# Kernel optimization log

Hardware: AMD Instinct MI355X
Metric: run time of the kernel (lower is better)

The kernel has to match this reference:

```python
import jax, jax.numpy as jnp
import numpy as np

NUM_TRAIN_PTS = 128
KNN = 32
KNN_CLEAN = 4
SIGMA = 0.01
FEAT_DIM = 128
B, N, M = 2, 40000, 40000


def knn_gather(query, pts, k):
    """Brute-force KNN. query [B,Q,3], pts [B,P,3] -> neighbors [B,Q,k,3]."""
    # squared euclidean distances [B,Q,P]
    d2 = (jnp.sum(query * query, -1, keepdims=True)
          - 2.0 * jnp.einsum('bqd,bpd->bqp', query, pts)
          + jnp.sum(pts * pts, -1)[:, None, :])
    _, idx = jax.lax.top_k(-d2, k)                # [B,Q,k]
    nn = jax.vmap(lambda p, i: p[i])(pts, idx)    # gather -> [B,Q,k,3]
    return nn


def setup_inputs() -> dict:
    key = jax.random.key(0)
    k0, k1, k2, k3, k4, k5 = jax.random.split(key, 6)
    noisy_pc = jax.random.uniform(k0, (B, N, 3), dtype=jnp.float32)
    clean_pc = jax.random.uniform(k1, (B, M, 3), dtype=jnp.float32)
    sampled_idx = jax.random.randint(k2, (NUM_TRAIN_PTS,), 0, N)
    Wf = jax.random.normal(k3, (3, FEAT_DIM), dtype=jnp.float32) * 0.1
    Wx = jax.random.normal(k4, (3, 3), dtype=jnp.float32) * 0.1
    Wc = jax.random.normal(k5, (FEAT_DIM, 3), dtype=jnp.float32) * 0.1
    return {'noisy_pc': noisy_pc, 'clean_pc': clean_pc, 'sampled_idx': sampled_idx,
            'Wf': Wf, 'Wx': Wx, 'Wc': Wc}


def reference(noisy_pc, clean_pc, sampled_idx, Wf, Wx, Wc):
    P, K, Kc = NUM_TRAIN_PTS, KNN, KNN_CLEAN
    # per-point feature extraction (stand-in for FeatureExtraction), then sample
    noisy_feat = jnp.einsum('bnd,df->bnf', noisy_pc, Wf)[:, sampled_idx, :]  # [B,P,F]
    q = noisy_pc[:, sampled_idx, :]                                          # [B,P,3]
    # first KNN: neighbors of sampled points within the noisy cloud
    f = knn_gather(q, noisy_pc, K)                                           # [B,P,K,3]
    # score network (stand-in): local offsets + conditioning feature
    estim_score = (jnp.einsum('bpkd,de->bpke', f - q[:, :, None, :], Wx)
                   + jnp.einsum('bpf,fe->bpe', noisy_feat, Wc)[:, :, None, :])  # [B,P,K,3]
    # second KNN: each neighbor point vs the clean cloud (clean shared per batch,
    # avoiding the torch .repeat of clean_pc per training point)
    knn_clean = knn_gather(f.reshape(f.shape[0], P * K, 3), clean_pc, Kc)
    knn_clean = knn_clean.reshape(f.shape[0], P, K, Kc, 3)                   # [B,P,K,Kc,3]
    ground_score = -jnp.mean(f[:, :, :, None, :] - knn_clean, axis=3)        # [B,P,K,3]
    loss = 0.5 * jnp.mean(jnp.sum((estim_score - ground_score) ** 2 * (1.0 / SIGMA), axis=-1))
    return loss
```

## Files before the change

kernel.cpp:

```cpp
#include <hip/hip_runtime.h>
#include <hip/hip_bf16.h>

#define N_PTS   40000
#define N_B     2
#define N_P     128
#define N_K     32
#define N_KC    4
#define N_FEAT  128
#define NQ2     (N_B * N_P * N_K)
#define BIGF    3.0e38f

#define K1SUB   8
#define K1RANGE (N_PTS / K1SUB)
#define QCAP1   512
#define LBUF1   320

#define QCAP    96

#define TAU2    4.0e-3f
#define TAU1    1.6e-2f

#define NG      15
#define NCELL   (NG * NG * NG)
#define GB_BLK  20
#define GB_PER  (N_PTS / GB_BLK)

#define NLOSSB  2048

__device__ int    g_sidx[N_P];
__device__ int    g_fidx[NQ2];
__device__ int    g_q1cnt[256];
__device__ unsigned long long g_q1list[256 * QCAP1];
__device__ int    g_bincnt[N_B * NCELL];
__device__ int    g_binstart[N_B * (NCELL + 1)];
__device__ int    g_cursor[N_B * NCELL];
__device__ float4 g_cpts[N_B * N_PTS];
__device__ int    g_cpidx[N_B * N_PTS];
__device__ float  g_lploss[NLOSSB];
__device__ float  g_M3[9];
__device__ float  g_WxS[9];

__device__ __forceinline__ int clampi(int v, int lo, int hi) { return v < lo ? lo : (v > hi ? hi : v); }

__device__ __forceinline__ unsigned long long packkey(float d, int idx)
{
    unsigned int u = __float_as_uint(d);
    u ^= (u >> 31) ? 0xFFFFFFFFu : 0x80000000u;
    return ((unsigned long long)u << 32) | (unsigned int)idx;
}

__device__ __forceinline__ int cell_of(float x, float y, float z)
{
    const int cx = clampi((int)(x * NG), 0, NG - 1);
    const int cy = clampi((int)(y * NG), 0, NG - 1);
    const int cz = clampi((int)(z * NG), 0, NG - 1);
    return cx + NG * (cy + NG * cz);
}

__global__ __launch_bounds__(256) void setup_kernel(
    const float* __restrict__ clean,
    const void*  __restrict__ sidx_raw,
    const float* __restrict__ Wf,
    const float* __restrict__ Wx,
    const float* __restrict__ Wc)
{
    __shared__ int hist[NCELL];
    __shared__ int flags[4];
    const int blk = blockIdx.x;
    const int tid = threadIdx.x;

    if (blk < N_B * GB_BLK) {
        const int bb = blk / GB_BLK;
        const int sb = blk % GB_BLK;
        const float* cb = clean + bb * (N_PTS * 3);

        for (int i = tid; i < NCELL; i += 256) hist[i] = 0;
        __syncthreads();

        const int j0 = sb * GB_PER;
        for (int j = j0 + tid; j < j0 + GB_PER; j += 256) {
            const float x = cb[j * 3 + 0], y = cb[j * 3 + 1], z = cb[j * 3 + 2];
            atomicAdd(&hist[cell_of(x, y, z)], 1);
        }
        __syncthreads();

        for (int i = tid; i < NCELL; i += 256) {
            const int v = hist[i];
            if (v) atomicAdd(&g_bincnt[bb * NCELL + i], v);
        }
    } else {
        if (tid < 9) {
            const int d = tid / 3, e = tid % 3;
            float acc = 0.0f;
            for (int f0 = 0; f0 < N_FEAT; ++f0)
                acc += Wf[d * N_FEAT + f0] * Wc[f0 * 3 + e];
            g_M3[tid]  = acc;
            g_WxS[tid] = Wx[tid];
        }
        if (tid == 0) { flags[0] = 1; flags[1] = 1; flags[2] = 1; flags[3] = 1; }
        __syncthreads();
        const int*       p32 = (const int*)sidx_raw;
        const long long* p64 = (const long long*)sidx_raw;
        const float*     pf  = (const float*)sidx_raw;
        if (tid < 128) {
            const int       v32 = p32[tid];
            const long long v64 = p64[tid];
            const float     vf  = pf[tid];
            if (!(v32 >= 0 && v32 < N_PTS)) atomicAnd(&flags[0], 0);
            if ((tid & 1) && v32 != 0)      atomicAnd(&flags[1], 0);
            if (!(v64 >= 0 && v64 < N_PTS)) atomicAnd(&flags[2], 0);
            if (!(vf >= 0.0f && vf < (float)N_PTS && vf == floorf(vf))) atomicAnd(&flags[3], 0);
        }
        __syncthreads();
        if (tid < 128) {
            int si;
            if (flags[0] && !(flags[1] && flags[2])) si = p32[tid];
            else if (flags[2])                       si = (int)p64[tid];
            else if (flags[3])                       si = (int)(pf[tid] + 0.5f);
            else                                     si = 0;
            g_sidx[tid] = clampi(si, 0, N_PTS - 1);
        }
    }
}

__global__ __launch_bounds__(256) void scan_knn1_kernel(
    const float* __restrict__ noisy)
{
    __shared__ unsigned long long buf[LBUF1];
    __shared__ int lcnt;
    __shared__ int base_s;
    __shared__ int wsum[4], woff[4];
    const int blk = blockIdx.x;
    const int tid = threadIdx.x;

    if (blk < N_B) {
        const int bb   = blk;
        const int lane = tid & 63, wv = tid >> 6;

        int lvals[14];
        int lsum = 0;
#pragma unroll
        for (int t = 0; t < 14; ++t) {
            const int idx = tid * 14 + t;
            lvals[t] = (idx < NCELL) ? g_bincnt[bb * NCELL + idx] : 0;
            lsum += lvals[t];
        }
        int v = lsum;
#pragma unroll
        for (int off = 1; off < 64; off <<= 1) {
            const int n = __shfl_up(v, off);
            if (lane >= off) v += n;
        }
        if (lane == 63) wsum[wv] = v;
        __syncthreads();
        if (tid == 0) { int r = 0; for (int w = 0; w < 4; ++w) { woff[w] = r; r += wsum[w]; } }
        __syncthreads();

        int run = woff[wv] + (v - lsum);
#pragma unroll
        for (int t = 0; t < 14; ++t) {
            const int idx = tid * 14 + t;
            if (idx < NCELL) {
                g_binstart[bb * (NCELL + 1) + idx] = run;
                g_cursor[bb * NCELL + idx] = run;
                g_bincnt[bb * NCELL + idx] = 0;
                run += lvals[t];
            }
        }
        if (tid == 0) g_binstart[bb * (NCELL + 1) + NCELL] = N_PTS;
    } else {
        const int idx = blk - N_B;
        const int qb  = idx & 255;
        const int sub = idx >> 8;
        const int b   = qb >> 7;
        const int p   = qb & 127;
        const float* nb = noisy + b * (N_PTS * 3);

        if (tid == 0) lcnt = 0;
        const int si = g_sidx[p];
        const float qx = nb[si * 3 + 0];
        const float qy = nb[si * 3 + 1];
        const float qz = nb[si * 3 + 2];
        __syncthreads();

        const int jbeg = sub * K1RANGE;
        const int jend = jbeg + K1RANGE;
        for (int j = jbeg + tid; j < jend; j += 256) {
            const float dx = qx - nb[j * 3 + 0];
            const float dy = qy - nb[j * 3 + 1];
            const float dz = qz - nb[j * 3 + 2];
            const float d2 = fmaf(dz, dz, fmaf(dy, dy, dx * dx));
            if (d2 < TAU1) {
                const int slot = atomicAdd(&lcnt, 1);
                if (slot < LBUF1)
                    buf[slot] = ((unsigned long long)__float_as_uint(d2) << 32) | (unsigned int)j;
            }
        }
        __syncthreads();

        const int cnt = lcnt;
        if (tid == 0) {
            const int add = (cnt <= LBUF1) ? cnt : (QCAP1 + 1000);
            base_s = atomicAdd(&g_q1cnt[qb], add);
        }
        __syncthreads();

        const int base = base_s;
        const int n = (cnt < LBUF1) ? cnt : LBUF1;
        for (int i = tid; i < n; i += 256) {
            const int o = base + i;
            if (o < QCAP1) g_q1list[qb * QCAP1 + o] = buf[i];
        }
    }
}

__global__ __launch_bounds__(256) void merge_scatter_kernel(
    const float* __restrict__ noisy,
    const float* __restrict__ clean)
{
    __shared__ unsigned long long keys[2048];
    const int blk = blockIdx.x;
    const int tid = threadIdx.x;

    if (blk >= 256) {
        const int idx = blk - 256;
        const int bb  = idx / GB_BLK;
        const int sb  = idx % GB_BLK;
        const float* cb = clean + bb * (N_PTS * 3);

        const int j0 = sb * GB_PER;
        for (int j = j0 + tid; j < j0 + GB_PER; j += 256) {
            const float x = cb[j * 3 + 0], y = cb[j * 3 + 1], z = cb[j * 3 + 2];
            const int c = cell_of(x, y, z);
            const int pos = atomicAdd(&g_cursor[bb * NCELL + c], 1);
            const float pp = fmaf(z, z, fmaf(y, y, x * x));
            g_cpts[bb * N_PTS + pos]  = make_float4(x, y, z, pp);
            g_cpidx[bb * N_PTS + pos] = j;
        }
        return;
    }

    const int qb  = blk;
    const int cnt = g_q1cnt[qb];

    if (cnt >= 32 && cnt <= QCAP1) {
        for (int i = tid; i < QCAP1; i += 256)
            keys[i] = (i < cnt) ? g_q1list[qb * QCAP1 + i] : ~0ULL;
        __syncthreads();
        for (int k = 2; k <= QCAP1; k <<= 1) {
            for (int jj = k >> 1; jj > 0; jj >>= 1) {
                const int idx = tid;
                const int i = ((idx & ~(jj - 1)) << 1) | (idx & (jj - 1));
                const int partner = i | jj;
                const bool asc = ((i & k) == 0);
                const unsigned long long a = keys[i];
                const unsigned long long c = keys[partner];
                if ((a > c) == asc) { keys[i] = c; keys[partner] = a; }
                __syncthreads();
            }
        }
    } else {
        const int b = qb >> 7;
        const float* nb = noisy + b * (N_PTS * 3);
        const int si = g_sidx[qb & 127];
        const float qx = nb[si * 3 + 0];
        const float qy = nb[si * 3 + 1];
        const float qz = nb[si * 3 + 2];

        float bd[8]; int bi[8];
#pragma unroll
        for (int i = 0; i < 8; ++i) { bd[i] = BIGF; bi[i] = 0x7fffffff; }
        for (int j = tid; j < N_PTS; j += 256) {
            const float dx = qx - nb[j * 3 + 0];
            const float dy = qy - nb[j * 3 + 1];
            const float dz = qz - nb[j * 3 + 2];
            const float d2 = fmaf(dz, dz, fmaf(dy, dy, dx * dx));
            if (d2 < bd[7]) {
                bd[7] = d2; bi[7] = j;
#pragma unroll
                for (int t = 7; t > 0; --t) {
                    if (bd[t] < bd[t - 1]) {
                        float td = bd[t]; bd[t] = bd[t - 1]; bd[t - 1] = td;
                        int   ti = bi[t]; bi[t] = bi[t - 1]; bi[t - 1] = ti;
                    }
                }
            }
        }
#pragma unroll
        for (int t = 0; t < 8; ++t)
            keys[tid * 8 + t] = ((unsigned long long)__float_as_uint(bd[t]) << 32)
                              | (unsigned int)bi[t];
        __syncthreads();
        for (int k = 2; k <= 2048; k <<= 1) {
            for (int jj = k >> 1; jj > 0; jj >>= 1) {
#pragma unroll
                for (int base = 0; base < 2048; base += 256) {
                    const int i = base + tid;
                    const int partner = i ^ jj;
                    if (partner > i) {
                        const bool asc = ((i & k) == 0);
                        const unsigned long long a = keys[i];
                        const unsigned long long c = keys[partner];
                        if ((a > c) == asc) { keys[i] = c; keys[partner] = a; }
                    }
                }
                __syncthreads();
            }
        }
    }

    if (tid < 32) {
        const int idx = (int)(keys[tid] & 0xFFFFFFFFull);
        g_fidx[qb * 32 + tid] = clampi(idx, 0, N_PTS - 1);
    }
    if (tid == 0) g_q1cnt[qb] = 0;
}

__global__ __launch_bounds__(256) void knn2_loss_kernel(
    const float* __restrict__ noisy,
    const float* __restrict__ clean)
{
    __shared__ float2 buf[4][QCAP];
    __shared__ int    bcnt[4];
    __shared__ float  red[4];
    const int tid  = threadIdx.x;
    const int wv   = tid >> 6;
    const int lane = tid & 63;
    const int g    = blockIdx.x * 4 + wv;
    const int b    = g >> 12;
    const int p    = (g >> 5) & 127;
    const float* nb = noisy + b * (N_PTS * 3);
    const float* cb = clean + b * (N_PTS * 3);

    if (lane == 0) bcnt[wv] = 0;

    const int fid = clampi(g_fidx[g], 0, N_PTS - 1);
    const float fx = nb[fid * 3 + 0];
    const float fy = nb[fid * 3 + 1];
    const float fz = nb[fid * 3 + 2];
    const float fm2x = -2.0f * fx, fm2y = -2.0f * fy, fm2z = -2.0f * fz;
    const float ff = fmaf(fz, fz, fmaf(fy, fy, fx * fx));
    const float taup = TAU2 - ff;

    const int cfx = clampi((int)(fx * NG), 0, NG - 1);
    const int cfy = clampi((int)(fy * NG), 0, NG - 1);
    const int cfz = clampi((int)(fz * NG), 0, NG - 1);
    const int bso = b * (NCELL + 1);
    const int bpo = b * N_PTS;

    if (lane < 27) {
        const int cx = cfx + (lane % 3) - 1;
        const int cy = cfy + ((lane / 3) % 3) - 1;
        const int cz = cfz + (lane / 9) - 1;
        if (cx >= 0 && cx < NG && cy >= 0 && cy < NG && cz >= 0 && cz < NG) {
            const int c = cx + NG * (cy + NG * cz);
            const int s = g_binstart[bso + c];
            const int e = g_binstart[bso + c + 1];
            for (int k = s; k < e; ++k) {
                const float4 pt = g_cpts[bpo + k];
                const float d2 = fmaf(fm2x, pt.x, fmaf(fm2y, pt.y, fmaf(fm2z, pt.z, pt.w)));
                if (d2 < taup) {
                    const int slot = atomicAdd(&bcnt[wv], 1);
                    if (slot < QCAP)
                        buf[wv][slot] = make_float2(d2, __int_as_float(g_cpidx[bpo + k]));
                }
            }
        }
    }
    __syncthreads();

    const int cnt = bcnt[wv];
    int nn[4];

    if (cnt >= 4 && cnt <= QCAP) {
        unsigned long long e0 = ~0ULL, e1 = ~0ULL;
        if (lane < cnt) {
            const float2 a = buf[wv][lane];
            e0 = packkey(a.x, __float_as_int(a.y));
        }
        if (lane + 64 < cnt) {
            const float2 a = buf[wv][lane + 64];
            e1 = packkey(a.x, __float_as_int(a.y));
        }
        if (e1 < e0) { unsigned long long t = e0; e0 = e1; e1 = t; }

        int c = 0;
#pragma unroll
        for (int r = 0; r < 4; ++r) {
            const unsigned long long h = (c == 0) ? e0 : ((c == 1) ? e1 : ~0ULL);
            unsigned long long m = h;
#pragma unroll
            for (int off = 32; off; off >>= 1) {
                const unsigned long long o = __shfl_xor(m, off);
                if (o < m) m = o;
            }
            if (h == m) c++;
            nn[r] = (int)(m & 0xFFFFFFFFull);
        }
    } else {
        float bd[4]; int bi[4];
#pragma unroll
        for (int t = 0; t < 4; ++t) { bd[t] = BIGF; bi[t] = 0x7fffffff; }
        for (int j = lane; j < N_PTS; j += 64) {
            const float dx = fx - cb[j * 3 + 0];
            const float dy = fy - cb[j * 3 + 1];
            const float dz = fz - cb[j * 3 + 2];
            const float d2 = fmaf(dz, dz, fmaf(dy, dy, dx * dx));
            if (d2 < bd[3]) {
                bd[3] = d2; bi[3] = j;
#pragma unroll
                for (int t = 3; t > 0; --t) {
                    if (bd[t] < bd[t - 1]) {
                        float td = bd[t]; bd[t] = bd[t - 1]; bd[t - 1] = td;
                        int   ti = bi[t]; bi[t] = bi[t - 1]; bi[t - 1] = ti;
                    }
                }
            }
        }
        int cur = 0;
        for (int r = 0; r < 4; ++r) {
            float v  = (cur < 4) ? bd[cur] : BIGF;
            int   vi = (cur < 4) ? bi[cur] : 0x7fffffff;
            int   who = lane;
#pragma unroll
            for (int off = 32; off; off >>= 1) {
                const float v2  = __shfl_down(v, off);
                const int   vi2 = __shfl_down(vi, off);
                const int   w2  = __shfl_down(who, off);
                if (v2 < v || (v2 == v && vi2 < vi)) { v = v2; vi = vi2; who = w2; }
            }
            const int bvi = __shfl(vi, 0);
            const int bwh = __shfl(who, 0);
            nn[r] = bvi;
            if (lane == bwh) cur++;
        }
    }

    float t2 = 0.0f;
    if (lane == 0) {
        const int si = g_sidx[p];
        const float qx = nb[si * 3 + 0], qy = nb[si * 3 + 1], qz = nb[si * 3 + 2];
        const int n0 = clampi(nn[0], 0, N_PTS - 1), n1 = clampi(nn[1], 0, N_PTS - 1);
        const int n2 = clampi(nn[2], 0, N_PTS - 1), n3 = clampi(nn[3], 0, N_PTS - 1);
        const float mx = 0.25f * (cb[n0*3+0] + cb[n1*3+0] + cb[n2*3+0] + cb[n3*3+0]);
        const float my = 0.25f * (cb[n0*3+1] + cb[n1*3+1] + cb[n2*3+1] + cb[n3*3+1]);
        const float mz = 0.25f * (cb[n0*3+2] + cb[n1*3+2] + cb[n2*3+2] + cb[n3*3+2]);

        const float gx = mx - fx, gy = my - fy, gz = mz - fz;
        const float rx = fx - qx, ry = fy - qy, rz = fz - qz;
        const float ex = rx * g_WxS[0] + ry * g_WxS[3] + rz * g_WxS[6] + qx * g_M3[0] + qy * g_M3[3] + qz * g_M3[6];
        const float ey = rx * g_WxS[1] + ry * g_WxS[4] + rz * g_WxS[7] + qx * g_M3[1] + qy * g_M3[4] + qz * g_M3[7];
        const float ez = rx * g_WxS[2] + ry * g_WxS[5] + rz * g_WxS[8] + qx * g_M3[2] + qy * g_M3[5] + qz * g_M3[8];
        const float dx = ex - gx, dy = ey - gy, dz = ez - gz;
        t2 = dx * dx + dy * dy + dz * dz;
    }

    if (lane == 0) red[wv] = t2;
    __syncthreads();
    if (tid == 0) g_lploss[blockIdx.x] = (red[0] + red[1]) + (red[2] + red[3]);
}

__global__ __launch_bounds__(256) void final_kernel(float* __restrict__ out)
{
    __shared__ float red[4];
    const int tid = threadIdx.x;
    float v = 0.0f;
    for (int i = tid; i < NLOSSB; i += 256) v += g_lploss[i];
#pragma unroll
    for (int off = 32; off; off >>= 1) v += __shfl_down(v, off);
    if ((tid & 63) == 0) red[tid >> 6] = v;
    __syncthreads();
    if (tid == 0) out[0] = ((red[0] + red[1]) + (red[2] + red[3])) * (50.0f / 8192.0f);
}

extern "C" void kernel_launch(void* const* d_in, const int* in_sizes, int n_in,
                              void* d_out, int out_size, void* d_ws, size_t ws_size,
                              hipStream_t stream)
{
    (void)d_ws; (void)ws_size; (void)in_sizes; (void)n_in; (void)out_size;

    const float* noisy = (const float*)d_in[0];
    const float* clean = (const float*)d_in[1];
    const float* Wf    = (const float*)d_in[3];
    const float* Wx    = (const float*)d_in[4];
    const float* Wc    = (const float*)d_in[5];

    setup_kernel<<<N_B * GB_BLK + 1, 256, 0, stream>>>(clean, d_in[2], Wf, Wx, Wc);
    scan_knn1_kernel<<<N_B + 256 * K1SUB, 256, 0, stream>>>(noisy);
    merge_scatter_kernel<<<256 + N_B * GB_BLK, 256, 0, stream>>>(noisy, clean);
    knn2_loss_kernel<<<NLOSSB, 256, 0, stream>>>(noisy, clean);
    final_kernel<<<1, 256, 0, stream>>>((float*)d_out);
}
```

Measured before the change: 112.4 us.

## Fuse pipeline stages using last-block-done atomics to cut kernel launches

Cuts the launch sequence from five kernels to three by using a global atomic counter in each stage, so the last finishing block does the follow-on work. The prefix scan of the grid histogram moves into the last histogram block, the per-query merge/sort into the last of its KNN1 sub-blocks, and the final loss reduction into the last knn2 block. This removes launch gaps and inter-kernel drains. In exchange it adds fences and atomics, and the last-block tails run serially on a single block.

Result: slower. 401.1 us (+257.0%).

```diff
diff --git a/kernel.cpp b/kernel.cpp
--- a/kernel.cpp
+++ b/kernel.cpp
@@ -39,6 +39,9 @@
 __device__ float  g_lploss[NLOSSB];
 __device__ float  g_M3[9];
 __device__ float  g_WxS[9];
+__device__ int    g_histdone[N_B];
+__device__ int    g_q1done[256];
+__device__ int    g_lossdone;
 
 __device__ __forceinline__ int clampi(int v, int lo, int hi) { return v < lo ? lo : (v > hi ? hi : v); }
 
@@ -66,6 +69,8 @@
 {
     __shared__ int hist[NCELL];
     __shared__ int flags[4];
+    __shared__ int wsum[4], woff[4];
+    __shared__ int islast;
     const int blk = blockIdx.x;
     const int tid = threadIdx.x;
 
@@ -87,6 +92,49 @@
         for (int i = tid; i < NCELL; i += 256) {
             const int v = hist[i];
             if (v) atomicAdd(&g_bincnt[bb * NCELL + i], v);
+        }
+
+        __threadfence();
+        __syncthreads();
+        if (tid == 0) islast = (atomicAdd(&g_histdone[bb], 1) == GB_BLK - 1);
+        __syncthreads();
+        if (!islast) return;
+        __threadfence();
+
+        const int lane = tid & 63, wv = tid >> 6;
+        int lvals[14];
+        int lsum = 0;
+#pragma unroll
+        for (int t = 0; t < 14; ++t) {
+            const int idx = tid * 14 + t;
+            lvals[t] = (idx < NCELL) ? g_bincnt[bb * NCELL + idx] : 0;
+            lsum += lvals[t];
+        }
+        int v = lsum;
+#pragma unroll
+        for (int off = 1; off < 64; off <<= 1) {
+            const int n = __shfl_up(v, off);
+            if (lane >= off) v += n;
+        }
+        if (lane == 63) wsum[wv] = v;
+        __syncthreads();
+        if (tid == 0) { int r = 0; for (int w = 0; w < 4; ++w) { woff[w] = r; r += wsum[w]; } }
+        __syncthreads();
+
+        int run = woff[wv] + (v - lsum);
+#pragma unroll
+        for (int t = 0; t < 14; ++t) {
+            const int idx = tid * 14 + t;
+            if (idx < NCELL) {
+                g_binstart[bb * (NCELL + 1) + idx] = run;
+                g_cursor[bb * NCELL + idx] = run;
+                g_bincnt[bb * NCELL + idx] = 0;
+                run += lvals[t];
+            }
+        }
+        if (tid == 0) {
+            g_binstart[bb * (NCELL + 1) + NCELL] = N_PTS;
+            g_histdone[bb] = 0;
         }
     } else {
         if (tid < 9) {
@@ -123,109 +171,18 @@
     }
 }
 
-__global__ __launch_bounds__(256) void scan_knn1_kernel(
-    const float* __restrict__ noisy)
-{
-    __shared__ unsigned long long buf[LBUF1];
-    __shared__ int lcnt;
-    __shared__ int base_s;
-    __shared__ int wsum[4], woff[4];
+__global__ __launch_bounds__(256) void knn1_scatter_kernel(
+    const float* __restrict__ noisy,
+    const float* __restrict__ clean)
+{
+    __shared__ unsigned long long skey[2048];
+    __shared__ int lcnt, base_s, islast;
     const int blk = blockIdx.x;
     const int tid = threadIdx.x;
 
-    if (blk < N_B) {
-        const int bb   = blk;
-        const int lane = tid & 63, wv = tid >> 6;
-
-        int lvals[14];
-        int lsum = 0;
-#pragma unroll
-        for (int t = 0; t < 14; ++t) {
-            const int idx = tid * 14 + t;
-            lvals[t] = (idx < NCELL) ? g_bincnt[bb * NCELL + idx] : 0;
-            lsum += lvals[t];
-        }
-        int v = lsum;
-#pragma unroll
-        for (int off = 1; off < 64; off <<= 1) {
-            const int n = __shfl_up(v, off);
-            if (lane >= off) v += n;
-        }
-        if (lane == 63) wsum[wv] = v;
-        __syncthreads();
-        if (tid == 0) { int r = 0; for (int w = 0; w < 4; ++w) { woff[w] = r; r += wsum[w]; } }
-        __syncthreads();
-
-        int run = woff[wv] + (v - lsum);
-#pragma unroll
-        for (int t = 0; t < 14; ++t) {
-            const int idx = tid * 14 + t;
-            if (idx < NCELL) {
-                g_binstart[bb * (NCELL + 1) + idx] = run;
-                g_cursor[bb * NCELL + idx] = run;
-                g_bincnt[bb * NCELL + idx] = 0;
-                run += lvals[t];
-            }
-        }
-        if (tid == 0) g_binstart[bb * (NCELL + 1) + NCELL] = N_PTS;
-    } else {
-        const int idx = blk - N_B;
-        const int qb  = idx & 255;
-        const int sub = idx >> 8;
-        const int b   = qb >> 7;
-        const int p   = qb & 127;
-        const float* nb = noisy + b * (N_PTS * 3);
-
-        if (tid == 0) lcnt = 0;
-        const int si = g_sidx[p];
-        const float qx = nb[si * 3 + 0];
-        const float qy = nb[si * 3 + 1];
-        const float qz = nb[si * 3 + 2];
-        __syncthreads();
-
-        const int jbeg = sub * K1RANGE;
-        const int jend = jbeg + K1RANGE;
-        for (int j = jbeg + tid; j < jend; j += 256) {
-            const float dx = qx - nb[j * 3 + 0];
-            const float dy = qy - nb[j * 3 + 1];
-            const float dz = qz - nb[j * 3 + 2];
-            const float d2 = fmaf(dz, dz, fmaf(dy, dy, dx * dx));
-            if (d2 < TAU1) {
-                const int slot = atomicAdd(&lcnt, 1);
-                if (slot < LBUF1)
-                    buf[slot] = ((unsigned long long)__float_as_uint(d2) << 32) | (unsigned int)j;
-            }
-        }
-        __syncthreads();
-
-        const int cnt = lcnt;
-        if (tid == 0) {
-            const int add = (cnt <= LBUF1) ? cnt : (QCAP1 + 1000);
-            base_s = atomicAdd(&g_q1cnt[qb], add);
-        }
-        __syncthreads();
-
-        const int base = base_s;
-        const int n = (cnt < LBUF1) ? cnt : LBUF1;
-        for (int i = tid; i < n; i += 256) {
-            const int o = base + i;
-            if (o < QCAP1) g_q1list[qb * QCAP1 + o] = buf[i];
-        }
-    }
-}
-
-__global__ __launch_bounds__(256) void merge_scatter_kernel(
-    const float* __restrict__ noisy,
-    const float* __restrict__ clean)
-{
-    __shared__ unsigned long long keys[2048];
-    const int blk = blockIdx.x;
-    const int tid = threadIdx.x;
-
-    if (blk >= 256) {
-        const int idx = blk - 256;
-        const int bb  = idx / GB_BLK;
-        const int sb  = idx % GB_BLK;
+    if (blk < N_B * GB_BLK) {
+        const int bb = blk / GB_BLK;
+        const int sb = blk % GB_BLK;
         const float* cb = clean + bb * (N_PTS * 3);
 
         const int j0 = sb * GB_PER;
@@ -240,33 +197,74 @@
         return;
     }
 
-    const int qb  = blk;
+    const int idx = blk - N_B * GB_BLK;
+    const int qb  = idx & 255;
+    const int sub = idx >> 8;
+    const int b   = qb >> 7;
+    const int p   = qb & 127;
+    const float* nb = noisy + b * (N_PTS * 3);
+
+    if (tid == 0) lcnt = 0;
+    const int si = g_sidx[p];
+    const float qx = nb[si * 3 + 0];
+    const float qy = nb[si * 3 + 1];
+    const float qz = nb[si * 3 + 2];
+    __syncthreads();
+
+    const int jbeg = sub * K1RANGE;
+    const int jend = jbeg + K1RANGE;
+    for (int j = jbeg + tid; j < jend; j += 256) {
+        const float dx = qx - nb[j * 3 + 0];
+        const float dy = qy - nb[j * 3 + 1];
+        const float dz = qz - nb[j * 3 + 2];
+        const float d2 = fmaf(dz, dz, fmaf(dy, dy, dx * dx));
+        if (d2 < TAU1) {
+            const int slot = atomicAdd(&lcnt, 1);
+            if (slot < LBUF1)
+                skey[slot] = ((unsigned long long)__float_as_uint(d2) << 32) | (unsigned int)j;
+        }
+    }
+    __syncthreads();
+
+    const int scnt = lcnt;
+    if (tid == 0) {
+        const int add = (scnt <= LBUF1) ? scnt : (QCAP1 + 1000);
+        base_s = atomicAdd(&g_q1cnt[qb], add);
+    }
+    __syncthreads();
+
+    const int base = base_s;
+    const int nout = (scnt < LBUF1) ? scnt : LBUF1;
+    for (int i = tid; i < nout; i += 256) {
+        const int o = base + i;
+        if (o < QCAP1) g_q1list[qb * QCAP1 + o] = skey[i];
+    }
+
+    __threadfence();
+    __syncthreads();
+    if (tid == 0) islast = (atomicAdd(&g_q1done[qb], 1) == K1SUB - 1);
+    __syncthreads();
+    if (!islast) return;
+    __threadfence();
+
     const int cnt = g_q1cnt[qb];
 
     if (cnt >= 32 && cnt <= QCAP1) {
         for (int i = tid; i < QCAP1; i += 256)
-            keys[i] = (i < cnt) ? g_q1list[qb * QCAP1 + i] : ~0ULL;
+            skey[i] = (i < cnt) ? g_q1list[qb * QCAP1 + i] : ~0ULL;
         __syncthreads();
         for (int k = 2; k <= QCAP1; k <<= 1) {
             for (int jj = k >> 1; jj > 0; jj >>= 1) {
-                const int idx = tid;
-                const int i = ((idx & ~(jj - 1)) << 1) | (idx & (jj - 1));
+                const int i = ((tid & ~(jj - 1)) << 1) | (tid & (jj - 1));
                 const int partner = i | jj;
                 const bool asc = ((i & k) == 0);
-                const unsigned long long a = keys[i];
-                const unsigned long long c = keys[partner];
-                if ((a > c) == asc) { keys[i] = c; keys[partner] = a; }
+                const unsigned long long a = skey[i];
+                const unsigned long long c = skey[partner];
+                if ((a > c) == asc) { skey[i] = c; skey[partner] = a; }
                 __syncthreads();
             }
         }
     } else {
-        const int b = qb >> 7;
-        const float* nb = noisy + b * (N_PTS * 3);
-        const int si = g_sidx[qb & 127];
-        const float qx = nb[si * 3 + 0];
-        const float qy = nb[si * 3 + 1];
-        const float qz = nb[si * 3 + 2];
-
         float bd[8]; int bi[8];
 #pragma unroll
         for (int i = 0; i < 8; ++i) { bd[i] = BIGF; bi[i] = 0x7fffffff; }
@@ -288,20 +286,20 @@
         }
 #pragma unroll
         for (int t = 0; t < 8; ++t)
-            keys[tid * 8 + t] = ((unsigned long long)__float_as_uint(bd[t]) << 32)
+            skey[tid * 8 + t] = ((unsigned long long)__float_as_uint(bd[t]) << 32)
                               | (unsigned int)bi[t];
         __syncthreads();
         for (int k = 2; k <= 2048; k <<= 1) {
             for (int jj = k >> 1; jj > 0; jj >>= 1) {
 #pragma unroll
-                for (int base = 0; base < 2048; base += 256) {
-                    const int i = base + tid;
+                for (int bas = 0; bas < 2048; bas += 256) {
+                    const int i = bas + tid;
                     const int partner = i ^ jj;
                     if (partner > i) {
                         const bool asc = ((i & k) == 0);
-                        const unsigned long long a = keys[i];
-                        const unsigned long long c = keys[partner];
-                        if ((a > c) == asc) { keys[i] = c; keys[partner] = a; }
+                        const unsigned long long a = skey[i];
+                        const unsigned long long c = skey[partner];
+                        if ((a > c) == asc) { skey[i] = c; skey[partner] = a; }
                     }
                 }
                 __syncthreads();
@@ -310,19 +308,21 @@
     }
 
     if (tid < 32) {
-        const int idx = (int)(keys[tid] & 0xFFFFFFFFull);
-        g_fidx[qb * 32 + tid] = clampi(idx, 0, N_PTS - 1);
-    }
-    if (tid == 0) g_q1cnt[qb] = 0;
+        const int fi = (int)(skey[tid] & 0xFFFFFFFFull);
+        g_fidx[qb * 32 + tid] = clampi(fi, 0, N_PTS - 1);
+    }
+    if (tid == 0) { g_q1cnt[qb] = 0; g_q1done[qb] = 0; }
 }
 
 __global__ __launch_bounds__(256) void knn2_loss_kernel(
     const float* __restrict__ noisy,
-    const float* __restrict__ clean)
+    const float* __restrict__ clean,
+    float* __restrict__ out)
 {
     __shared__ float2 buf[4][QCAP];
     __shared__ int    bcnt[4];
     __shared__ float  red[4];
+    __shared__ int    islast;
     const int tid  = threadIdx.x;
     const int wv   = tid >> 6;
     const int lane = tid & 63;
@@ -458,19 +458,24 @@
     if (lane == 0) red[wv] = t2;
     __syncthreads();
     if (tid == 0) g_lploss[blockIdx.x] = (red[0] + red[1]) + (red[2] + red[3]);
-}
-
-__global__ __launch_bounds__(256) void final_kernel(float* __restrict__ out)
-{
-    __shared__ float red[4];
-    const int tid = threadIdx.x;
+
+    __threadfence();
+    __syncthreads();
+    if (tid == 0) islast = (atomicAdd(&g_lossdone, 1) == NLOSSB - 1);
+    __syncthreads();
+    if (!islast) return;
+    __threadfence();
+
     float v = 0.0f;
     for (int i = tid; i < NLOSSB; i += 256) v += g_lploss[i];
 #pragma unroll
     for (int off = 32; off; off >>= 1) v += __shfl_down(v, off);
     if ((tid & 63) == 0) red[tid >> 6] = v;
     __syncthreads();
-    if (tid == 0) out[0] = ((red[0] + red[1]) + (red[2] + red[3])) * (50.0f / 8192.0f);
+    if (tid == 0) {
+        out[0] = ((red[0] + red[1]) + (red[2] + red[3])) * (50.0f / 8192.0f);
+        g_lossdone = 0;
+    }
 }
 
 extern "C" void kernel_launch(void* const* d_in, const int* in_sizes, int n_in,
@@ -486,8 +491,6 @@
     const float* Wc    = (const float*)d_in[5];
 
     setup_kernel<<<N_B * GB_BLK + 1, 256, 0, stream>>>(clean, d_in[2], Wf, Wx, Wc);
-    scan_knn1_kernel<<<N_B + 256 * K1SUB, 256, 0, stream>>>(noisy);
-    merge_scatter_kernel<<<256 + N_B * GB_BLK, 256, 0, stream>>>(noisy, clean);
-    knn2_loss_kernel<<<NLOSSB, 256, 0, stream>>>(noisy, clean);
-    final_kernel<<<1, 256, 0, stream>>>((float*)d_out);
-}
+    knn1_scatter_kernel<<<N_B * GB_BLK + 256 * K1SUB, 256, 0, stream>>>(noisy, clean);
+    knn2_loss_kernel<<<NLOSSB, 256, 0, stream>>>(noisy, clean, (float*)d_out);
+}
```

## Replace brute-force KNN1 scan and prefix-sum binning with fixed-capacity grid buckets

Applied to the files above, without the earlier changes.

Builds a coarse 7^3 grid over the noisy cloud and fixed-capacity buckets for the clean-cloud grid with direct atomic slot insertion, replacing the histogram plus prefix-scan plus scatter pipeline. The first KNN now scans only the 27 neighbouring coarse cells instead of all 40000 points, and candidate selection is fused into the same kernel, removing one launch and the global candidate list. Counter resets move into extra blocks of the final kernel. The change relies on bucket capacities not overflowing; when they do, it falls back to the existing slower paths.

Result: no change. 114.3 us (+1.8%).

```diff
diff --git a/kernel.cpp b/kernel.cpp
--- a/kernel.cpp
+++ b/kernel.cpp
@@ -10,11 +10,7 @@
 #define NQ2     (N_B * N_P * N_K)
 #define BIGF    3.0e38f
 
-#define K1SUB   8
-#define K1RANGE (N_PTS / K1SUB)
 #define QCAP1   512
-#define LBUF1   320
-
 #define QCAP    96
 
 #define TAU2    4.0e-3f
@@ -22,6 +18,12 @@
 
 #define NG      15
 #define NCELL   (NG * NG * NG)
+#define CAPC    32
+
+#define NG1     7
+#define NCELL1  (NG1 * NG1 * NG1)
+#define CAP1N   192
+
 #define GB_BLK  20
 #define GB_PER  (N_PTS / GB_BLK)
 
@@ -29,13 +31,11 @@
 
 __device__ int    g_sidx[N_P];
 __device__ int    g_fidx[NQ2];
-__device__ int    g_q1cnt[256];
-__device__ unsigned long long g_q1list[256 * QCAP1];
-__device__ int    g_bincnt[N_B * NCELL];
-__device__ int    g_binstart[N_B * (NCELL + 1)];
-__device__ int    g_cursor[N_B * NCELL];
-__device__ float4 g_cpts[N_B * N_PTS];
-__device__ int    g_cpidx[N_B * N_PTS];
+__device__ int    g_ncnt[N_B * NCELL1];
+__device__ float4 g_npts[N_B * NCELL1 * CAP1N];
+__device__ int    g_ccnt[N_B * NCELL];
+__device__ float4 g_cpts[N_B * NCELL * CAPC];
+__device__ int    g_cpidx[N_B * NCELL * CAPC];
 __device__ float  g_lploss[NLOSSB];
 __device__ float  g_M3[9];
 __device__ float  g_WxS[9];
@@ -57,14 +57,14 @@
     return cx + NG * (cy + NG * cz);
 }
 
-__global__ __launch_bounds__(256) void setup_kernel(
+__global__ __launch_bounds__(256) void build_kernel(
+    const float* __restrict__ noisy,
     const float* __restrict__ clean,
     const void*  __restrict__ sidx_raw,
     const float* __restrict__ Wf,
     const float* __restrict__ Wx,
     const float* __restrict__ Wc)
 {
-    __shared__ int hist[NCELL];
     __shared__ int flags[4];
     const int blk = blockIdx.x;
     const int tid = threadIdx.x;
@@ -72,21 +72,33 @@
     if (blk < N_B * GB_BLK) {
         const int bb = blk / GB_BLK;
         const int sb = blk % GB_BLK;
+        const float* nb = noisy + bb * (N_PTS * 3);
+        const int j0 = sb * GB_PER;
+        for (int j = j0 + tid; j < j0 + GB_PER; j += 256) {
+            const float x = nb[j * 3 + 0], y = nb[j * 3 + 1], z = nb[j * 3 + 2];
+            const int cx = clampi((int)(x * NG1), 0, NG1 - 1);
+            const int cy = clampi((int)(y * NG1), 0, NG1 - 1);
+            const int cz = clampi((int)(z * NG1), 0, NG1 - 1);
+            const int ci = bb * NCELL1 + cx + NG1 * (cy + NG1 * cz);
+            const int pos = atomicAdd(&g_ncnt[ci], 1);
+            if (pos < CAP1N)
+                g_npts[ci * CAP1N + pos] = make_float4(x, y, z, __int_as_float(j));
+        }
+    } else if (blk < 2 * N_B * GB_BLK) {
+        const int blk2 = blk - N_B * GB_BLK;
+        const int bb = blk2 / GB_BLK;
+        const int sb = blk2 % GB_BLK;
         const float* cb = clean + bb * (N_PTS * 3);
-
-        for (int i = tid; i < NCELL; i += 256) hist[i] = 0;
-        __syncthreads();
-
         const int j0 = sb * GB_PER;
         for (int j = j0 + tid; j < j0 + GB_PER; j += 256) {
             const float x = cb[j * 3 + 0], y = cb[j * 3 + 1], z = cb[j * 3 + 2];
-            atomicAdd(&hist[cell_of(x, y, z)], 1);
-        }
-        __syncthreads();
-
-        for (int i = tid; i < NCELL; i += 256) {
-            const int v = hist[i];
-            if (v) atomicAdd(&g_bincnt[bb * NCELL + i], v);
+            const int ci = bb * NCELL + cell_of(x, y, z);
+            const int pos = atomicAdd(&g_ccnt[ci], 1);
+            if (pos < CAPC) {
+                const float pp = fmaf(z, z, fmaf(y, y, x * x));
+                g_cpts[ci * CAPC + pos]  = make_float4(x, y, z, pp);
+                g_cpidx[ci * CAPC + pos] = j;
+            }
         }
     } else {
         if (tid < 9) {
@@ -123,134 +135,63 @@
     }
 }
 
-__global__ __launch_bounds__(256) void scan_knn1_kernel(
+__global__ __launch_bounds__(256) void knn1_grid_kernel(
     const float* __restrict__ noisy)
 {
-    __shared__ unsigned long long buf[LBUF1];
-    __shared__ int lcnt;
-    __shared__ int base_s;
-    __shared__ int wsum[4], woff[4];
-    const int blk = blockIdx.x;
-    const int tid = threadIdx.x;
-
-    if (blk < N_B) {
-        const int bb   = blk;
-        const int lane = tid & 63, wv = tid >> 6;
-
-        int lvals[14];
-        int lsum = 0;
-#pragma unroll
-        for (int t = 0; t < 14; ++t) {
-            const int idx = tid * 14 + t;
-            lvals[t] = (idx < NCELL) ? g_bincnt[bb * NCELL + idx] : 0;
-            lsum += lvals[t];
-        }
-        int v = lsum;
-#pragma unroll
-        for (int off = 1; off < 64; off <<= 1) {
-            const int n = __shfl_up(v, off);
-            if (lane >= off) v += n;
-        }
-        if (lane == 63) wsum[wv] = v;
-        __syncthreads();
-        if (tid == 0) { int r = 0; for (int w = 0; w < 4; ++w) { woff[w] = r; r += wsum[w]; } }
-        __syncthreads();
-
-        int run = woff[wv] + (v - lsum);
-#pragma unroll
-        for (int t = 0; t < 14; ++t) {
-            const int idx = tid * 14 + t;
-            if (idx < NCELL) {
-                g_binstart[bb * (NCELL + 1) + idx] = run;
-                g_cursor[bb * NCELL + idx] = run;
-                g_bincnt[bb * NCELL + idx] = 0;
-                run += lvals[t];
-            }
-        }
-        if (tid == 0) g_binstart[bb * (NCELL + 1) + NCELL] = N_PTS;
-    } else {
-        const int idx = blk - N_B;
-        const int qb  = idx & 255;
-        const int sub = idx >> 8;
-        const int b   = qb >> 7;
-        const int p   = qb & 127;
-        const float* nb = noisy + b * (N_PTS * 3);
-
-        if (tid == 0) lcnt = 0;
-        const int si = g_sidx[p];
-        const float qx = nb[si * 3 + 0];
-        const float qy = nb[si * 3 + 1];
-        const float qz = nb[si * 3 + 2];
-        __syncthreads();
-
-        const int jbeg = sub * K1RANGE;
-        const int jend = jbeg + K1RANGE;
-        for (int j = jbeg + tid; j < jend; j += 256) {
-            const float dx = qx - nb[j * 3 + 0];
-            const float dy = qy - nb[j * 3 + 1];
-            const float dz = qz - nb[j * 3 + 2];
+    __shared__ unsigned long long keys[2048];
+    __shared__ int lcnt, ovf;
+    const int qb   = blockIdx.x;
+    const int tid  = threadIdx.x;
+    const int wv   = tid >> 6;
+    const int lane = tid & 63;
+    const int b    = qb >> 7;
+    const int p    = qb & 127;
+    const float* nb = noisy + b * (N_PTS * 3);
+
+    if (tid == 0) { lcnt = 0; ovf = 0; }
+    const int si = g_sidx[p];
+    const float qx = nb[si * 3 + 0];
+    const float qy = nb[si * 3 + 1];
+    const float qz = nb[si * 3 + 2];
+    const int c1x = clampi((int)(qx * NG1), 0, NG1 - 1);
+    const int c1y = clampi((int)(qy * NG1), 0, NG1 - 1);
+    const int c1z = clampi((int)(qz * NG1), 0, NG1 - 1);
+    __syncthreads();
+
+    for (int i = wv; i < 27; i += 4) {
+        const int cx = c1x + (i % 3) - 1;
+        const int cy = c1y + ((i / 3) % 3) - 1;
+        const int cz = c1z + (i / 9) - 1;
+        if (cx < 0 || cx >= NG1 || cy < 0 || cy >= NG1 || cz < 0 || cz >= NG1) continue;
+        const int ci  = b * NCELL1 + cx + NG1 * (cy + NG1 * cz);
+        const int cnt = g_ncnt[ci];
+        if (cnt > CAP1N && lane == 0) ovf = 1;
+        const int n = (cnt < CAP1N) ? cnt : CAP1N;
+        const float4* bp = &g_npts[ci * CAP1N];
+        for (int k = lane; k < n; k += 64) {
+            const float4 pt = bp[k];
+            const float dx = qx - pt.x;
+            const float dy = qy - pt.y;
+            const float dz = qz - pt.z;
             const float d2 = fmaf(dz, dz, fmaf(dy, dy, dx * dx));
             if (d2 < TAU1) {
                 const int slot = atomicAdd(&lcnt, 1);
-                if (slot < LBUF1)
-                    buf[slot] = ((unsigned long long)__float_as_uint(d2) << 32) | (unsigned int)j;
-            }
-        }
-        __syncthreads();
-
-        const int cnt = lcnt;
-        if (tid == 0) {
-            const int add = (cnt <= LBUF1) ? cnt : (QCAP1 + 1000);
-            base_s = atomicAdd(&g_q1cnt[qb], add);
-        }
-        __syncthreads();
-
-        const int base = base_s;
-        const int n = (cnt < LBUF1) ? cnt : LBUF1;
-        for (int i = tid; i < n; i += 256) {
-            const int o = base + i;
-            if (o < QCAP1) g_q1list[qb * QCAP1 + o] = buf[i];
-        }
-    }
-}
-
-__global__ __launch_bounds__(256) void merge_scatter_kernel(
-    const float* __restrict__ noisy,
-    const float* __restrict__ clean)
-{
-    __shared__ unsigned long long keys[2048];
-    const int blk = blockIdx.x;
-    const int tid = threadIdx.x;
-
-    if (blk >= 256) {
-        const int idx = blk - 256;
-        const int bb  = idx / GB_BLK;
-        const int sb  = idx % GB_BLK;
-        const float* cb = clean + bb * (N_PTS * 3);
-
-        const int j0 = sb * GB_PER;
-        for (int j = j0 + tid; j < j0 + GB_PER; j += 256) {
-            const float x = cb[j * 3 + 0], y = cb[j * 3 + 1], z = cb[j * 3 + 2];
-            const int c = cell_of(x, y, z);
-            const int pos = atomicAdd(&g_cursor[bb * NCELL + c], 1);
-            const float pp = fmaf(z, z, fmaf(y, y, x * x));
-            g_cpts[bb * N_PTS + pos]  = make_float4(x, y, z, pp);
-            g_cpidx[bb * N_PTS + pos] = j;
-        }
-        return;
-    }
-
-    const int qb  = blk;
-    const int cnt = g_q1cnt[qb];
-
-    if (cnt >= 32 && cnt <= QCAP1) {
+                if (slot < QCAP1)
+                    keys[slot] = ((unsigned long long)__float_as_uint(d2) << 32)
+                               | (unsigned int)__float_as_int(pt.w);
+            }
+        }
+    }
+    __syncthreads();
+
+    const int cnt = lcnt;
+    if (!ovf && cnt >= 32 && cnt <= QCAP1) {
         for (int i = tid; i < QCAP1; i += 256)
-            keys[i] = (i < cnt) ? g_q1list[qb * QCAP1 + i] : ~0ULL;
+            if (i >= cnt) keys[i] = ~0ULL;
         __syncthreads();
         for (int k = 2; k <= QCAP1; k <<= 1) {
             for (int jj = k >> 1; jj > 0; jj >>= 1) {
-                const int idx = tid;
-                const int i = ((idx & ~(jj - 1)) << 1) | (idx & (jj - 1));
+                const int i = ((tid & ~(jj - 1)) << 1) | (tid & (jj - 1));
                 const int partner = i | jj;
                 const bool asc = ((i & k) == 0);
                 const unsigned long long a = keys[i];
@@ -260,13 +201,6 @@
             }
         }
     } else {
-        const int b = qb >> 7;
-        const float* nb = noisy + b * (N_PTS * 3);
-        const int si = g_sidx[qb & 127];
-        const float qx = nb[si * 3 + 0];
-        const float qy = nb[si * 3 + 1];
-        const float qz = nb[si * 3 + 2];
-
         float bd[8]; int bi[8];
 #pragma unroll
         for (int i = 0; i < 8; ++i) { bd[i] = BIGF; bi[i] = 0x7fffffff; }
@@ -313,7 +247,6 @@
         const int idx = (int)(keys[tid] & 0xFFFFFFFFull);
         g_fidx[qb * 32 + tid] = clampi(idx, 0, N_PTS - 1);
     }
-    if (tid == 0) g_q1cnt[qb] = 0;
 }
 
 __global__ __launch_bounds__(256) void knn2_loss_kernel(
@@ -345,27 +278,37 @@
     const int cfx = clampi((int)(fx * NG), 0, NG - 1);
     const int cfy = clampi((int)(fy * NG), 0, NG - 1);
     const int cfz = clampi((int)(fz * NG), 0, NG - 1);
-    const int bso = b * (NCELL + 1);
-    const int bpo = b * N_PTS;
-
+
+    int cnt_l = 0, base_l = 0;
     if (lane < 27) {
         const int cx = cfx + (lane % 3) - 1;
         const int cy = cfy + ((lane / 3) % 3) - 1;
         const int cz = cfz + (lane / 9) - 1;
         if (cx >= 0 && cx < NG && cy >= 0 && cy < NG && cz >= 0 && cz < NG) {
-            const int c = cx + NG * (cy + NG * cz);
-            const int s = g_binstart[bso + c];
-            const int e = g_binstart[bso + c + 1];
-            for (int k = s; k < e; ++k) {
-                const float4 pt = g_cpts[bpo + k];
+            const int ci = b * NCELL + cx + NG * (cy + NG * cz);
+            cnt_l  = g_ccnt[ci];
+            base_l = ci * CAPC;
+        }
+    }
+    const unsigned long long ovfm = __ballot(lane < 27 && cnt_l > CAPC);
+    if (ovfm == 0ULL) {
+        for (int t = lane; t < 27 * CAPC; t += 64) {
+            const int ci = t >> 5;
+            const int sl = t & (CAPC - 1);
+            const int cc  = __shfl(cnt_l, ci);
+            const int cb2 = __shfl(base_l, ci);
+            if (sl < cc) {
+                const float4 pt = g_cpts[cb2 + sl];
                 const float d2 = fmaf(fm2x, pt.x, fmaf(fm2y, pt.y, fmaf(fm2z, pt.z, pt.w)));
                 if (d2 < taup) {
                     const int slot = atomicAdd(&bcnt[wv], 1);
                     if (slot < QCAP)
-                        buf[wv][slot] = make_float2(d2, __int_as_float(g_cpidx[bpo + k]));
+                        buf[wv][slot] = make_float2(d2, __int_as_float(g_cpidx[cb2 + sl]));
                 }
             }
         }
+    } else if (lane == 0) {
+        bcnt[wv] = QCAP + 1000;
     }
     __syncthreads();
 
@@ -464,6 +407,16 @@
 {
     __shared__ float red[4];
     const int tid = threadIdx.x;
+
+    if (blockIdx.x == 1) {
+        for (int i = tid; i < N_B * NCELL; i += 256) g_ccnt[i] = 0;
+        return;
+    }
+    if (blockIdx.x == 2) {
+        for (int i = tid; i < N_B * NCELL1; i += 256) g_ncnt[i] = 0;
+        return;
+    }
+
     float v = 0.0f;
     for (int i = tid; i < NLOSSB; i += 256) v += g_lploss[i];
 #pragma unroll
@@ -485,9 +438,8 @@
     const float* Wx    = (const float*)d_in[4];
     const float* Wc    = (const float*)d_in[5];
 
-    setup_kernel<<<N_B * GB_BLK + 1, 256, 0, stream>>>(clean, d_in[2], Wf, Wx, Wc);
-    scan_knn1_kernel<<<N_B + 256 * K1SUB, 256, 0, stream>>>(noisy);
-    merge_scatter_kernel<<<256 + N_B * GB_BLK, 256, 0, stream>>>(noisy, clean);
+    build_kernel<<<2 * N_B * GB_BLK + 1, 256, 0, stream>>>(noisy, clean, d_in[2], Wf, Wx, Wc);
+    knn1_grid_kernel<<<256, 256, 0, stream>>>(noisy);
     knn2_loss_kernel<<<NLOSSB, 256, 0, stream>>>(noisy, clean);
-    final_kernel<<<1, 256, 0, stream>>>((float*)d_out);
-}
+    final_kernel<<<3, 256, 0, stream>>>((float*)d_out);
+}
```
